# Optimization experiments

Measured on AMD Instinct MI355X. Metric: run time of the kernel, lower is better.

Reference implementation:

```python
import jax, jax.numpy as jnp
import numpy as np

EMBED_DIM = 1024
NUM_HEADS = 16
HEAD_DIM = EMBED_DIM // NUM_HEADS
BSZ, TGT, SRC = 4, 1024, 2048


def setup_inputs() -> dict:
    key = jax.random.key(0)
    ks = jax.random.split(key, 12)
    init = 1.0 / np.sqrt(EMBED_DIM)
    return {
        "hidden_states": jax.random.normal(ks[0], (BSZ, TGT, EMBED_DIM), jnp.float32),
        "key_value_states": jax.random.normal(ks[1], (BSZ, SRC, EMBED_DIM), jnp.float32),
        "bias": jax.random.normal(ks[2], (BSZ, NUM_HEADS, TGT, SRC), jnp.float32),
        "Wq": jax.random.normal(ks[3], (EMBED_DIM, EMBED_DIM), jnp.float32) * init,
        "bq": jax.random.normal(ks[4], (EMBED_DIM,), jnp.float32) * init,
        "Wk": jax.random.normal(ks[5], (EMBED_DIM, EMBED_DIM), jnp.float32) * init,
        "bk": jax.random.normal(ks[6], (EMBED_DIM,), jnp.float32) * init,
        "Wv": jax.random.normal(ks[7], (EMBED_DIM, EMBED_DIM), jnp.float32) * init,
        "bv": jax.random.normal(ks[8], (EMBED_DIM,), jnp.float32) * init,
        "Wo": jax.random.normal(ks[9], (EMBED_DIM, EMBED_DIM), jnp.float32) * init,
        "bo": jax.random.normal(ks[10], (EMBED_DIM,), jnp.float32) * init,
    }


def reference(hidden_states, key_value_states, bias, Wq, bq, Wk, bk, Wv, bv, Wo, bo):
    B, T, E = hidden_states.shape
    S = key_value_states.shape[1]
    H, hd = NUM_HEADS, HEAD_DIM
    scaling = hd ** (-0.5)
    # torch Linear: y = x @ W^T + b
    q = (hidden_states @ Wq.T + bq) * scaling            # [B,T,E]
    k = key_value_states @ Wk.T + bk                     # [B,S,E]
    v = key_value_states @ Wv.T + bv                     # [B,S,E]
    q = q.reshape(B, T, H, hd).transpose(0, 2, 1, 3)     # [B,H,T,hd]
    k = k.reshape(B, S, H, hd).transpose(0, 2, 1, 3)     # [B,H,S,hd]
    v = v.reshape(B, S, H, hd).transpose(0, 2, 1, 3)     # [B,H,S,hd]
    scores = jnp.einsum('bhtd,bhsd->bhts', q, k) + bias  # [B,H,T,S]
    probs = jax.nn.softmax(scores, axis=-1)
    attn = jnp.einsum('bhts,bhsd->bhtd', probs, v)       # [B,H,T,hd]
    # Faithful to the original: reshape (B*H, T, hd) -> (B, T, E) WITHOUT
    # transposing heads back (this is how the torch source does it).
    attn = attn.reshape(B, T, E)
    return attn @ Wo.T + bo
```

## Files before the change

### kernel.cpp

```cpp
#include <hip/hip_runtime.h>

#define DEVI __device__ __forceinline__

typedef __attribute__((ext_vector_type(4))) float f32x4;
typedef __attribute__((ext_vector_type(8))) short bf16x8;

DEVI unsigned short f2bf(float f) {
  unsigned int u = __builtin_bit_cast(unsigned int, f);
  u += 0x7FFFu + ((u >> 16) & 1u);
  return (unsigned short)(u >> 16);
}

DEVI void load_lds16(const void* g, void* l) {
  __builtin_amdgcn_global_load_lds(
      (__attribute__((address_space(1))) void*)g,
      (__attribute__((address_space(3))) void*)l,
      16, 0, 0);
}

DEVI int xcd_swz(int bid, int chunk) { return (bid & 7) * chunk + (bid >> 3); }

struct CvtArgs {
  const float* src[6];
  unsigned short* dst[6];
  int cum[6];
};

__global__ __launch_bounds__(256) void cvt_all(CvtArgs a, int total4) {
  int i = blockIdx.x * 256 + threadIdx.x;
  if (i >= total4) return;
  int s = 0;
#pragma unroll
  for (int k = 1; k < 6; ++k) s += (i >= a.cum[k]);
  const int j = i - a.cum[s];
  const float4 v = reinterpret_cast<const float4*>(a.src[s])[j];
  ushort4 o;
  o.x = f2bf(v.x); o.y = f2bf(v.y); o.z = f2bf(v.z); o.w = f2bf(v.w);
  reinterpret_cast<ushort4*>(a.dst[s])[j] = o;
}

template<bool OUT_BF16>
DEVI void gemm_core(const unsigned short* __restrict__ A,
                    const unsigned short* __restrict__ W,
                    const float* __restrict__ bias,
                    void* __restrict__ out,
                    float scale, int log2R,
                    long sb, long st, long sh, long sd,
                    int bx, int by, bool vt)
{
  constexpr int K = 1024;
  __shared__ unsigned short smem[2 * 128 * 64];
  unsigned short* As = smem;
  unsigned short* Bs = smem + 8192;

  const int tid  = threadIdx.x;
  const int wid  = tid >> 6;
  const int lane = tid & 63;
  const int m0 = bx * 128;
  const int n0 = by * 128;
  const int wr = (wid >> 1) * 64;
  const int wc = (wid & 1) * 64;
  const int lg = lane >> 4;
  const int ll = lane & 15;

  f32x4 acc[4][4] = {};

  const char* Ab = (const char*)A + (long)m0 * K * 2;
  const char* Wb = (const char*)W + (long)n0 * K * 2;
  char* AsB = (char*)As;
  char* BsB = (char*)Bs;
  const long rowstride = (long)K * 2;

  for (int kt = 0; kt < K; kt += 64) {
#pragma unroll
    for (int j = 0; j < 4; ++j) {
      const int o    = (wid * 4 + j) * 1024 + lane * 16;
      const int row  = o >> 7;
      const int colb = o & 127;
      load_lds16(Ab + (long)row * rowstride + (long)kt * 2 + colb, AsB + (wid * 4 + j) * 1024);
      load_lds16(Wb + (long)row * rowstride + (long)kt * 2 + colb, BsB + (wid * 4 + j) * 1024);
    }
    __syncthreads();
#pragma unroll
    for (int ks = 0; ks < 2; ++ks) {
      bf16x8 af[4], bfr[4];
#pragma unroll
      for (int i = 0; i < 4; ++i) {
        af[i]  = *(const bf16x8*)&As[(wr + i * 16 + ll) * 64 + ks * 32 + lg * 8];
        bfr[i] = *(const bf16x8*)&Bs[(wc + i * 16 + ll) * 64 + ks * 32 + lg * 8];
      }
#pragma unroll
      for (int i = 0; i < 4; ++i)
#pragma unroll
        for (int j = 0; j < 4; ++j)
          acc[i][j] = __builtin_amdgcn_mfma_f32_16x16x32_bf16(af[i], bfr[j], acc[i][j], 0, 0, 0);
    }
    __syncthreads();
  }

  if (OUT_BF16 && vt) {
    const int m_base = m0 + wr;
    const int b  = m_base >> log2R;
    const int tb = m_base & ((1 << log2R) - 1);
    unsigned short* Tw = smem + wid * 2176;
#pragma unroll
    for (int h2 = 0; h2 < 2; ++h2) {
#pragma unroll
      for (int jj = 0; jj < 2; ++jj) {
        const int j = h2 * 2 + jj;
        const float bj = bias[n0 + wc + j * 16 + ll];
#pragma unroll
        for (int i = 0; i < 4; ++i)
#pragma unroll
          for (int r = 0; r < 4; ++r)
            Tw[(jj * 16 + ll) * 68 + i * 16 + lg * 4 + r] = f2bf((acc[i][j][r] + bj) * scale);
      }
      asm volatile("s_waitcnt lgkmcnt(0)" ::: "memory");
#pragma unroll
      for (int k = 0; k < 8; ++k) {
        const int dloc = k * 4 + (lane >> 4);
        const int t4   = (lane & 15) * 4;
        const ushort4 vv = *(const ushort4*)&Tw[dloc * 68 + t4];
        const int n = n0 + wc + h2 * 32 + dloc;
        const int h = n >> 6, dd = n & 63;
        *(ushort4*)((unsigned short*)out + (long)b * sb + (long)h * sh + (long)dd * sd + tb + t4) = vv;
      }
      if (h2 == 0) asm volatile("s_waitcnt lgkmcnt(0)" ::: "memory");
    }
    return;
  }

  const int Rmask = (1 << log2R) - 1;
#pragma unroll
  for (int j = 0; j < 4; ++j) {
    const int n = n0 + wc + j * 16 + ll;
    const float bj = bias[n];
    const int h = n >> 6, d = n & 63;
#pragma unroll
    for (int i = 0; i < 4; ++i) {
      const int mb = m0 + wr + i * 16 + lg * 4;
#pragma unroll
      for (int r = 0; r < 4; ++r) {
        const int m = mb + r;
        const int b = m >> log2R;
        const int t = m & Rmask;
        const long off = (long)b * sb + (long)t * st + (long)h * sh + (long)d * sd;
        const float v = (acc[i][j][r] + bj) * scale;
        if (OUT_BF16) ((unsigned short*)out)[off] = f2bf(v);
        else          ((float*)out)[off] = v;
      }
    }
  }
}

struct GemmDesc {
  const unsigned short* A;
  const unsigned short* W;
  const float* bias;
  unsigned short* out;
  float scale;
  int log2R;
  long sb, st, sh, sd;
};

__global__ __launch_bounds__(256) void gemm_qkv(GemmDesc d0, GemmDesc d1, GemmDesc d2) {
  int bid = xcd_swz(blockIdx.x, 160);
  const GemmDesc* d;
  bool vt = false;
  if (bid < 256)      { d = &d0; }
  else if (bid < 768) { d = &d1; bid -= 256; }
  else                { d = &d2; bid -= 768; vt = true; }
  gemm_core<true>(d->A, d->W, d->bias, d->out, d->scale, d->log2R,
                  d->sb, d->st, d->sh, d->sd, bid >> 3, bid & 7, vt);
}

__global__ __launch_bounds__(256) void gemm_o(
    const unsigned short* __restrict__ A,
    const unsigned short* __restrict__ W,
    const float* __restrict__ bias,
    float* __restrict__ out,
    long sb, long st, long sh, long sd)
{
  const int bid = xcd_swz(blockIdx.x, 32);
  gemm_core<false>(A, W, bias, out, 1.0f, 10, sb, st, sh, sd, bid >> 3, bid & 7, false);
}

__global__ __launch_bounds__(256, 4) void attn_fused(
    const unsigned short* __restrict__ Qb,
    const unsigned short* __restrict__ Kb,
    const unsigned short* __restrict__ Vt,
    const float* __restrict__ bias,
    unsigned short* __restrict__ Ob)
{
  constexpr int T = 1024, S = 2048;
  __shared__ unsigned short Ks[64 * 72];
  __shared__ unsigned short Vs[64 * 72];
  __shared__ unsigned short Ps[4][16 * 72];

  const int tid = threadIdx.x;
  const int w = tid >> 6, lane = tid & 63;
  const int lg = lane >> 4, ll = lane & 15;

  const int wg = xcd_swz(blockIdx.x, 128);
  const int bh = wg >> 4;
  const int tt = wg & 15;
  const int t0 = tt * 64;
  const int trow = t0 + w * 16;

  bf16x8 qf[2];
#pragma unroll
  for (int ks = 0; ks < 2; ++ks)
    qf[ks] = *(const bf16x8*)(Qb + ((long)bh * T + trow + ll) * 64 + ks * 32 + lg * 8);

  f32x4 acc[4] = {};
  float m_run = -1e30f, l_run = 0.0f;

  const char* Kg = (const char*)(Kb + (long)bh * S * 64);
  const char* Vg = (const char*)(Vt + (long)bh * 64 * S);
  const float* biasg = bias + ((long)bh * T + t0) * S;
  const float* bias_row = biasg + (long)(w * 16 + ll) * S + lg * 4;

  for (int sc = 0; sc < S / 64; ++sc) {
#pragma unroll
    for (int r2 = 0; r2 < 2; ++r2) {
      const int o = (tid + r2 * 256) * 16;
      const int row = o >> 7, colb = o & 127;
      uint4 kd = *(const uint4*)(Kg + (long)(sc * 64 + row) * 128 + colb);
      *(uint4*)((char*)&Ks[0] + row * 144 + colb) = kd;
      uint4 vd = *(const uint4*)(Vg + (long)row * (S * 2) + sc * 128 + colb);
      *(uint4*)((char*)&Vs[0] + row * 144 + colb) = vd;
    }
    __syncthreads();

    f32x4 sv[4] = {};
#pragma unroll
    for (int ks = 0; ks < 2; ++ks) {
      bf16x8 kf[4];
#pragma unroll
      for (int sf = 0; sf < 4; ++sf)
        kf[sf] = *(const bf16x8*)((const char*)&Ks[0] + (sf * 16 + ll) * 144 + (ks * 32 + lg * 8) * 2);
#pragma unroll
      for (int sf = 0; sf < 4; ++sf)
        sv[sf] = __builtin_amdgcn_mfma_f32_16x16x32_bf16(kf[sf], qf[ks], sv[sf], 0, 0, 0);
    }

    const float* bp = bias_row + sc * 64;
#pragma unroll
    for (int sf = 0; sf < 4; ++sf) {
      const float4 b4 = *(const float4*)(bp + sf * 16);
      sv[sf][0] += b4.x; sv[sf][1] += b4.y; sv[sf][2] += b4.z; sv[sf][3] += b4.w;
    }

    float cm = sv[0][0];
#pragma unroll
    for (int sf = 0; sf < 4; ++sf)
#pragma unroll
      for (int r = 0; r < 4; ++r) cm = fmaxf(cm, sv[sf][r]);
    cm = fmaxf(cm, __shfl_xor(cm, 16));
    cm = fmaxf(cm, __shfl_xor(cm, 32));

    const float mnew = fmaxf(m_run, cm);
    const float alpha = __expf(m_run - mnew);
    float ps = 0.0f;
#pragma unroll
    for (int sf = 0; sf < 4; ++sf)
#pragma unroll
      for (int r = 0; r < 4; ++r) {
        const float p = __expf(sv[sf][r] - mnew);
        sv[sf][r] = p;
        ps += p;
      }
    ps += __shfl_xor(ps, 16);
    ps += __shfl_xor(ps, 32);
    l_run = l_run * alpha + ps;
    m_run = mnew;

    float ar[4];
#pragma unroll
    for (int r = 0; r < 4; ++r) ar[r] = __shfl(alpha, lg * 4 + r);
#pragma unroll
    for (int df = 0; df < 4; ++df)
#pragma unroll
      for (int r = 0; r < 4; ++r) acc[df][r] *= ar[r];

    unsigned short* Pw = &Ps[w][0];
#pragma unroll
    for (int sf = 0; sf < 4; ++sf) {
      ushort4 pw;
      pw.x = f2bf(sv[sf][0]); pw.y = f2bf(sv[sf][1]);
      pw.z = f2bf(sv[sf][2]); pw.w = f2bf(sv[sf][3]);
      *(ushort4*)&Pw[ll * 72 + sf * 16 + lg * 4] = pw;
    }
    asm volatile("s_waitcnt lgkmcnt(0)" ::: "memory");
    __builtin_amdgcn_sched_barrier(0);

#pragma unroll
    for (int ks = 0; ks < 2; ++ks) {
      bf16x8 pa = *(const bf16x8*)((const char*)Pw + ll * 144 + ks * 64 + lg * 16);
      bf16x8 vf[4];
#pragma unroll
      for (int df = 0; df < 4; ++df)
        vf[df] = *(const bf16x8*)((const char*)&Vs[0] + (df * 16 + ll) * 144 + (ks * 32 + lg * 8) * 2);
#pragma unroll
      for (int df = 0; df < 4; ++df)
        acc[df] = __builtin_amdgcn_mfma_f32_16x16x32_bf16(pa, vf[df], acc[df], 0, 0, 0);
    }
    __syncthreads();
  }

  const float inv = 1.0f / l_run;
  float ir[4];
#pragma unroll
  for (int r = 0; r < 4; ++r) ir[r] = __shfl(inv, lg * 4 + r);
#pragma unroll
  for (int df = 0; df < 4; ++df)
#pragma unroll
    for (int r = 0; r < 4; ++r) {
      const long oo = ((long)bh * T + trow + lg * 4 + r) * 64 + df * 16 + ll;
      Ob[oo] = f2bf(acc[df][r] * ir[r]);
    }
}

extern "C" void kernel_launch(void* const* d_in, const int* in_sizes, int n_in,
                              void* d_out, int out_size, void* d_ws, size_t ws_size,
                              hipStream_t stream) {
  constexpr int B = 4, T = 1024, S = 2048, E = 1024;
  const float* hs   = (const float*)d_in[0];
  const float* kv   = (const float*)d_in[1];
  const float* bias = (const float*)d_in[2];
  const float* Wq   = (const float*)d_in[3];
  const float* bq   = (const float*)d_in[4];
  const float* Wk   = (const float*)d_in[5];
  const float* bk   = (const float*)d_in[6];
  const float* Wv   = (const float*)d_in[7];
  const float* bv   = (const float*)d_in[8];
  const float* Wo   = (const float*)d_in[9];
  const float* bo   = (const float*)d_in[10];

  char* ws = (char*)d_ws;
  const size_t MB = 1024 * 1024;
  unsigned short* hs_bf = (unsigned short*)(ws);
  unsigned short* kv_bf = (unsigned short*)(ws + 8 * MB);
  unsigned short* wq_bf = (unsigned short*)(ws + 24 * MB);
  unsigned short* wk_bf = (unsigned short*)(ws + 26 * MB);
  unsigned short* wv_bf = (unsigned short*)(ws + 28 * MB);
  unsigned short* wo_bf = (unsigned short*)(ws + 30 * MB);
  unsigned short* q_buf = (unsigned short*)(ws + 32 * MB);
  unsigned short* k_buf = (unsigned short*)(ws + 40 * MB);
  unsigned short* v_buf = (unsigned short*)(ws + 56 * MB);
  unsigned short* a_buf = (unsigned short*)(ws + 72 * MB);

  CvtArgs ca;
  ca.src[0] = hs;  ca.dst[0] = hs_bf;
  ca.src[1] = kv;  ca.dst[1] = kv_bf;
  ca.src[2] = Wq;  ca.dst[2] = wq_bf;
  ca.src[3] = Wk;  ca.dst[3] = wk_bf;
  ca.src[4] = Wv;  ca.dst[4] = wv_bf;
  ca.src[5] = Wo;  ca.dst[5] = wo_bf;
  const int n4_hs = B * T * E / 4, n4_kv = B * S * E / 4, n4_w = E * E / 4;
  ca.cum[0] = 0;
  ca.cum[1] = n4_hs;
  ca.cum[2] = n4_hs + n4_kv;
  ca.cum[3] = n4_hs + n4_kv + n4_w;
  ca.cum[4] = n4_hs + n4_kv + 2 * n4_w;
  ca.cum[5] = n4_hs + n4_kv + 3 * n4_w;
  const int total4 = n4_hs + n4_kv + 4 * n4_w;
  cvt_all<<<dim3((total4 + 255) / 256), dim3(256), 0, stream>>>(ca, total4);

  GemmDesc dq{hs_bf, wq_bf, bq, q_buf, 0.125f, 10,
              (long)T * E, 64L, (long)T * 64, 1L};
  GemmDesc dk{kv_bf, wk_bf, bk, k_buf, 1.0f, 11,
              (long)S * E, 64L, (long)S * 64, 1L};
  GemmDesc dv{kv_bf, wv_bf, bv, v_buf, 1.0f, 11,
              (long)S * E, 1L, (long)S * 64, (long)S};
  gemm_qkv<<<dim3(1280), 256, 0, stream>>>(dq, dk, dv);

  attn_fused<<<dim3(1024), 256, 0, stream>>>(q_buf, k_buf, v_buf, bias, a_buf);

  gemm_o<<<dim3(256), 256, 0, stream>>>(
      a_buf, wo_bf, bo, (float*)d_out,
      (long)T * E, (long)E, 64L, 1L);
}
```

Before: 306.3 us.

## Stage GEMM epilogues through LDS, use nontemporal loads, prefetch attention bias

The GEMM epilogue for the non-transposed bf16 and the fp32 outputs now transposes each warp's tile through LDS, so global stores become contiguous ushort4/float2 row writes instead of scattered scalar stores. The fp32 conversion kernel and the attention bias reads use nontemporal loads so streamed data does not pollute cache. The bias tile for each attention chunk is issued before the K/V LDS staging so its latency overlaps the QK^T MFMAs. This adds LDS traffic and waitcnt barriers in the epilogue and keeps more registers live in the attention loop.

```diff
diff --git a/kernel.cpp b/kernel.cpp
--- a/kernel.cpp
+++ b/kernel.cpp
@@ -33,9 +33,9 @@
 #pragma unroll
   for (int k = 1; k < 6; ++k) s += (i >= a.cum[k]);
   const int j = i - a.cum[s];
-  const float4 v = reinterpret_cast<const float4*>(a.src[s])[j];
+  const f32x4 v = __builtin_nontemporal_load((const f32x4*)a.src[s] + j);
   ushort4 o;
-  o.x = f2bf(v.x); o.y = f2bf(v.y); o.z = f2bf(v.z); o.w = f2bf(v.w);
+  o.x = f2bf(v[0]); o.y = f2bf(v[1]); o.z = f2bf(v[2]); o.w = f2bf(v[3]);
   reinterpret_cast<ushort4*>(a.dst[s])[j] = o;
 }
 
@@ -98,57 +98,90 @@
     __syncthreads();
   }
 
+  const int Rmask  = (1 << log2R) - 1;
+  const int m_base = m0 + wr;
+  const int b   = m_base >> log2R;
+  const int tbs = m_base & Rmask;
+  const int nn  = n0 + wc;
+  float bj[4];
+#pragma unroll
+  for (int j = 0; j < 4; ++j) bj[j] = bias[nn + j * 16 + ll];
+
   if (OUT_BF16 && vt) {
-    const int m_base = m0 + wr;
-    const int b  = m_base >> log2R;
-    const int tb = m_base & ((1 << log2R) - 1);
     unsigned short* Tw = smem + wid * 2176;
 #pragma unroll
     for (int h2 = 0; h2 < 2; ++h2) {
 #pragma unroll
       for (int jj = 0; jj < 2; ++jj) {
         const int j = h2 * 2 + jj;
-        const float bj = bias[n0 + wc + j * 16 + ll];
 #pragma unroll
         for (int i = 0; i < 4; ++i)
 #pragma unroll
           for (int r = 0; r < 4; ++r)
-            Tw[(jj * 16 + ll) * 68 + i * 16 + lg * 4 + r] = f2bf((acc[i][j][r] + bj) * scale);
+            Tw[(jj * 16 + ll) * 68 + i * 16 + lg * 4 + r] = f2bf((acc[i][j][r] + bj[j]) * scale);
       }
       asm volatile("s_waitcnt lgkmcnt(0)" ::: "memory");
 #pragma unroll
       for (int k = 0; k < 8; ++k) {
-        const int dloc = k * 4 + (lane >> 4);
-        const int t4   = (lane & 15) * 4;
+        const int dloc = k * 4 + lg;
+        const int t4   = ll * 4;
         const ushort4 vv = *(const ushort4*)&Tw[dloc * 68 + t4];
-        const int n = n0 + wc + h2 * 32 + dloc;
+        const int n = nn + h2 * 32 + dloc;
         const int h = n >> 6, dd = n & 63;
-        *(ushort4*)((unsigned short*)out + (long)b * sb + (long)h * sh + (long)dd * sd + tb + t4) = vv;
+        *(ushort4*)((unsigned short*)out + (long)b * sb + (long)h * sh + (long)dd * sd + tbs + t4) = vv;
       }
       if (h2 == 0) asm volatile("s_waitcnt lgkmcnt(0)" ::: "memory");
     }
     return;
   }
 
-  const int Rmask = (1 << log2R) - 1;
-#pragma unroll
-  for (int j = 0; j < 4; ++j) {
-    const int n = n0 + wc + j * 16 + ll;
-    const float bj = bias[n];
-    const int h = n >> 6, d = n & 63;
+  if (OUT_BF16) {
+    const int h = nn >> 6;
+    unsigned short* ob = (unsigned short*)out + (long)b * sb + (long)h * sh;
+    unsigned short* Tw = smem + wid * 2176;
+#pragma unroll
+    for (int p = 0; p < 2; ++p) {
+#pragma unroll
+      for (int i2 = 0; i2 < 2; ++i2) {
+        const int i = p * 2 + i2;
+#pragma unroll
+        for (int j = 0; j < 4; ++j)
+#pragma unroll
+          for (int r = 0; r < 4; ++r)
+            Tw[(i2 * 16 + lg * 4 + r) * 68 + j * 16 + ll] = f2bf((acc[i][j][r] + bj[j]) * scale);
+      }
+      asm volatile("s_waitcnt lgkmcnt(0)" ::: "memory");
+#pragma unroll
+      for (int k = 0; k < 8; ++k) {
+        const int t_loc = k * 4 + lg;
+        const int d4    = ll * 4;
+        const ushort4 vv = *(const ushort4*)&Tw[t_loc * 68 + d4];
+        *(ushort4*)(ob + (long)(tbs + p * 32 + t_loc) * st + d4) = vv;
+      }
+      if (p == 0) asm volatile("s_waitcnt lgkmcnt(0)" ::: "memory");
+    }
+    return;
+  }
+
+  {
+    float* ob = (float*)out + (long)b * sb + nn;
+    float* TwF = (float*)smem + wid * 1056;
 #pragma unroll
     for (int i = 0; i < 4; ++i) {
-      const int mb = m0 + wr + i * 16 + lg * 4;
-#pragma unroll
-      for (int r = 0; r < 4; ++r) {
-        const int m = mb + r;
-        const int b = m >> log2R;
-        const int t = m & Rmask;
-        const long off = (long)b * sb + (long)t * st + (long)h * sh + (long)d * sd;
-        const float v = (acc[i][j][r] + bj) * scale;
-        if (OUT_BF16) ((unsigned short*)out)[off] = f2bf(v);
-        else          ((float*)out)[off] = v;
-      }
+#pragma unroll
+      for (int j = 0; j < 4; ++j)
+#pragma unroll
+        for (int r = 0; r < 4; ++r)
+          TwF[(lg * 4 + r) * 66 + j * 16 + ll] = acc[i][j][r] + bj[j];
+      asm volatile("s_waitcnt lgkmcnt(0)" ::: "memory");
+#pragma unroll
+      for (int k = 0; k < 8; ++k) {
+        const int t_loc = k * 2 + (lane >> 5);
+        const int c2    = (lane & 31) * 2;
+        const float2 v = *(const float2*)&TwF[t_loc * 66 + c2];
+        *(float2*)(ob + (long)(tbs + i * 16 + t_loc) * st + c2) = v;
+      }
+      if (i < 3) asm volatile("s_waitcnt lgkmcnt(0)" ::: "memory");
     }
   }
 }
@@ -221,6 +254,12 @@
   const float* bias_row = biasg + (long)(w * 16 + ll) * S + lg * 4;
 
   for (int sc = 0; sc < S / 64; ++sc) {
+    const float* bp = bias_row + sc * 64;
+    f32x4 b4[4];
+#pragma unroll
+    for (int sf = 0; sf < 4; ++sf)
+      b4[sf] = __builtin_nontemporal_load((const f32x4*)(bp + sf * 16));
+
 #pragma unroll
     for (int r2 = 0; r2 < 2; ++r2) {
       const int o = (tid + r2 * 256) * 16;
@@ -244,11 +283,10 @@
         sv[sf] = __builtin_amdgcn_mfma_f32_16x16x32_bf16(kf[sf], qf[ks], sv[sf], 0, 0, 0);
     }
 
-    const float* bp = bias_row + sc * 64;
 #pragma unroll
     for (int sf = 0; sf < 4; ++sf) {
-      const float4 b4 = *(const float4*)(bp + sf * 16);
-      sv[sf][0] += b4.x; sv[sf][1] += b4.y; sv[sf][2] += b4.z; sv[sf][3] += b4.w;
+      sv[sf][0] += b4[sf][0]; sv[sf][1] += b4[sf][1];
+      sv[sf][2] += b4[sf][2]; sv[sf][3] += b4[sf][3];
     }
 
     float cm = sv[0][0];
```

After: 277.3 us. 1.1x faster.
